# Performance work log

Hardware: AMD Instinct MI355X
Metric: run time of the kernel (lower is better)

## Reference

```python
import jax, jax.numpy as jnp
import numpy as np

H = 512          # hidden_size
B = 1024         # batch
T = 256          # warmup sequence length
NUM_STEPS = 64


def setup_inputs() -> dict:
    key = jax.random.key(0)
    ks = jax.random.split(key, 8)
    bound = 1.0 / np.sqrt(H)  # torch default init for RNN/Linear
    x = jax.random.normal(ks[0], (B, T), dtype=jnp.float32)
    W_ih = jax.random.uniform(ks[1], (H, 1), jnp.float32, -bound, bound)
    W_hh = jax.random.uniform(ks[2], (H, H), jnp.float32, -bound, bound)
    b_ih = jax.random.uniform(ks[3], (H,), jnp.float32, -bound, bound)
    b_hh = jax.random.uniform(ks[4], (H,), jnp.float32, -bound, bound)
    W_fc = jax.random.uniform(ks[5], (1, H), jnp.float32, -bound, bound)
    b_fc = jax.random.uniform(ks[6], (1,), jnp.float32, -bound, bound)
    return {"x": x, "W_ih": W_ih, "W_hh": W_hh, "b_ih": b_ih,
            "b_hh": b_hh, "W_fc": W_fc, "b_fc": b_fc, "num_steps": NUM_STEPS}


def reference(x, W_ih, W_hh, b_ih, b_hh, W_fc, b_fc, num_steps):
    # Phase 1: warmup RNN over the input series. h_t = relu(x_t*W_ih + b_ih + h@W_hh^T + b_hh)
    bias = b_ih + b_hh  # [H]
    w_in = W_ih[:, 0]   # [H], input_size == 1

    def warm_step(h, xt):                      # h: [B,H], xt: [B]
        h = jax.nn.relu(xt[:, None] * w_in[None, :] + h @ W_hh.T + bias)
        return h, None

    h0 = jnp.zeros((B, H), dtype=x.dtype)
    h, _ = jax.lax.scan(warm_step, h0, x.T)    # scan over time: x.T is [T,B]

    def roll_step(h, _):
        y = h @ W_fc.T + b_fc                  # [B,1]
        h = jax.nn.relu(y @ W_ih.T + h @ W_hh.T + bias)
        return h, y

    _, ys = jax.lax.scan(roll_step, h, None, length=num_steps)  # ys: [S,B,1]
    return jnp.transpose(ys, (1, 0, 2))        # [B, num_steps, 1]
```

## Files before the change

kernel.cpp:

```cpp
#include <hip/hip_runtime.h>
#include <stdint.h>

#define H 512
#define B_SZ 1024
#define T_WARM 256
#define NSTEPS 64
#define TOTAL_T (T_WARM + NSTEPS)

#define RPB 16
#define HC 128
#define NTEAM 64
#define NCG 4
#define NBLK 256
#define NTHR 512
#define HSTR 520

typedef __attribute__((ext_vector_type(8))) short bf16x8;
typedef __attribute__((ext_vector_type(4))) float f32x4;

__device__ __forceinline__ ushort f2bf(float f) {
    uint32_t u = __builtin_bit_cast(uint32_t, f);
    u += 0x7FFFu + ((u >> 16) & 1u);
    return (ushort)(u >> 16);
}
__device__ __forceinline__ float bf2f(ushort h) {
    uint32_t u = ((uint32_t)h) << 16;
    return __builtin_bit_cast(float, u);
}

__global__ void prep_kernel(const float* __restrict__ x,
                            const float* __restrict__ W_hh,
                            const float* __restrict__ b_ih,
                            const float* __restrict__ b_hh,
                            ushort* __restrict__ Wh, ushort* __restrict__ Wl,
                            float* __restrict__ bias, float* __restrict__ xT,
                            uint32_t* __restrict__ Hb0, uint32_t* __restrict__ flags) {
    int i = blockIdx.x * NTHR + threadIdx.x;
    Hb0[i] = 0u;
    if (i < 4096) flags[i] = 0u;
    if (i < H * H) {
        float w = W_hh[i];
        ushort hi = f2bf(w);
        float rem = w - bf2f(hi);
        Wh[i] = hi;
        Wl[i] = f2bf(rem);
    }
    if (i < B_SZ * T_WARM) {
        int b = i & (B_SZ - 1), t = i >> 10;
        xT[t * B_SZ + b] = x[b * T_WARM + t];
    }
    if (i < H) bias[i] = b_ih[i] + b_hh[i];
}

__global__ __launch_bounds__(NTHR, 1)
void rnn_kernel(const float* __restrict__ xT,
                const float* __restrict__ W_ih,
                const float* __restrict__ b_fc_p,
                const float* __restrict__ W_fc,
                const ushort* __restrict__ Wh_g,
                const ushort* __restrict__ Wl_g,
                const float* __restrict__ bias_g,
                uint32_t* __restrict__ Hb0, uint32_t* __restrict__ Hb1,
                uint32_t* __restrict__ flags,
                float* __restrict__ out) {
    __shared__ ushort h_hi[RPB * HSTR];
    __shared__ ushort h_lo[RPB * HSTR];
    __shared__ float w_fc_s[H];
    __shared__ float w_in_s[HC];
    __shared__ float bias_s[HC];
    __shared__ float sx[RPB];
    __shared__ float sy[RPB];

    const int tid = threadIdx.x;
    const int bid = blockIdx.x;
    const int team = bid & (NTEAM - 1);
    const int cg = bid >> 6;
    const int row0 = team * RPB;
    const int col0 = cg * HC;

    w_fc_s[tid & (H - 1)] = W_fc[tid & (H - 1)];
    if (tid < HC) { w_in_s[tid] = W_ih[col0 + tid]; bias_s[tid] = bias_g[col0 + tid]; }
    const float bfc = b_fc_p[0];

    const int lane = tid & 63;
    const int wv = tid >> 6;
    const int n = lane & 15, q = lane >> 4;

    bf16x8 Bh[16], Bl[16];
    {
        const ushort* wh = Wh_g + (col0 + wv * 16 + n) * H + q * 8;
        const ushort* wl = Wl_g + (col0 + wv * 16 + n) * H + q * 8;
        #pragma unroll
        for (int kt = 0; kt < 16; ++kt) {
            Bh[kt] = *(const bf16x8*)(wh + kt * 32);
            Bl[kt] = *(const bf16x8*)(wl + kt * 32);
        }
    }

    uint32_t* myflag = flags + (team * NCG + cg) * 16;
    const uint32_t* pollflag = flags + (team * NCG + (wv >> 1)) * 16;

    for (int t = 0; t < TOTAL_T; ++t) {
        float xv = 0.f;
        if (t < T_WARM && tid < RPB) xv = xT[t * B_SZ + row0 + tid];

        if (t > 0) {
            while (__hip_atomic_load(pollflag, __ATOMIC_RELAXED, __HIP_MEMORY_SCOPE_AGENT)
                   < (uint32_t)t)
                __builtin_amdgcn_s_sleep(1);
        }

        uint64_t tmp[8];
        {
            const uint32_t* hb = (t & 1) ? Hb1 : Hb0;
            const uint64_t* src = (const uint64_t*)hb;
            #pragma unroll
            for (int it = 0; it < 8; ++it) {
                int idx = it * 64 + lane;
                int r = idx >> 5, cpair = idx & 31;
                tmp[it] = __hip_atomic_load(src + ((row0 + r) * 256 + wv * 32 + cpair),
                                            __ATOMIC_RELAXED, __HIP_MEMORY_SCOPE_AGENT);
            }
        }
        __syncthreads();

        #pragma unroll
        for (int it = 0; it < 8; ++it) {
            int idx = it * 64 + lane;
            int r = idx >> 5, cpair = idx & 31;
            int k = wv * 64 + cpair * 2;
            uint64_t u = tmp[it];
            uint32_t w0 = (uint32_t)u, w1 = (uint32_t)(u >> 32);
            uint32_t hw = (w0 >> 16) | (w1 & 0xFFFF0000u);
            uint32_t lw = (w0 & 0xFFFFu) | (w1 << 16);
            *(uint32_t*)(&h_hi[r * HSTR + k]) = hw;
            *(uint32_t*)(&h_lo[r * HSTR + k]) = lw;
        }
        if (t < T_WARM && tid < RPB) sx[tid] = xv;
        __syncthreads();

        if (t >= T_WARM) {
            if (tid < RPB * 16) {
                int r = tid >> 4, seg = tid & 15;
                const ushort* hh = &h_hi[r * HSTR];
                const ushort* hl = &h_lo[r * HSTR];
                float s = 0.f;
                #pragma unroll
                for (int kk = 0; kk < 32; ++kk) {
                    int k = seg + kk * 16;
                    s += (bf2f(hh[k]) + bf2f(hl[k])) * w_fc_s[k];
                }
                #pragma unroll
                for (int off = 8; off; off >>= 1) s += __shfl_down(s, off, 16);
                if (seg == 0) {
                    float y = s + bfc;
                    sy[r] = y;
                    if (cg == 0) out[(row0 + r) * NSTEPS + (t - T_WARM)] = y;
                }
            }
            __syncthreads();
        }

        f32x4 acc0 = {0.f, 0.f, 0.f, 0.f}, acc1 = {0.f, 0.f, 0.f, 0.f};
        const ushort* ha = &h_hi[n * HSTR] + q * 8;
        const ushort* la = &h_lo[n * HSTR] + q * 8;
        #pragma unroll
        for (int kt = 0; kt < 16; kt += 2) {
            {
                bf16x8 ah = *(const bf16x8*)(ha + kt * 32);
                bf16x8 al = *(const bf16x8*)(la + kt * 32);
                acc0 = __builtin_amdgcn_mfma_f32_16x16x32_bf16(ah, Bh[kt], acc0, 0, 0, 0);
                acc0 = __builtin_amdgcn_mfma_f32_16x16x32_bf16(al, Bh[kt], acc0, 0, 0, 0);
                acc0 = __builtin_amdgcn_mfma_f32_16x16x32_bf16(ah, Bl[kt], acc0, 0, 0, 0);
            }
            {
                bf16x8 ah = *(const bf16x8*)(ha + (kt + 1) * 32);
                bf16x8 al = *(const bf16x8*)(la + (kt + 1) * 32);
                acc1 = __builtin_amdgcn_mfma_f32_16x16x32_bf16(ah, Bh[kt + 1], acc1, 0, 0, 0);
                acc1 = __builtin_amdgcn_mfma_f32_16x16x32_bf16(al, Bh[kt + 1], acc1, 0, 0, 0);
                acc1 = __builtin_amdgcn_mfma_f32_16x16x32_bf16(ah, Bl[kt + 1], acc1, 0, 0, 0);
            }
        }

        const int jl = wv * 16 + n;
        const float wi = w_in_s[jl], bj = bias_s[jl];
        uint32_t* dst = ((t & 1) ? Hb0 : Hb1) + col0 + jl;
        #pragma unroll
        for (int i = 0; i < 4; ++i) {
            int m = q * 4 + i;
            float sv = (t < T_WARM) ? sx[m] : sy[m];
            float v = acc0[i] + acc1[i] + sv * wi + bj;
            v = fmaxf(v, 0.f);
            ushort hi = f2bf(v);
            float rem = v - bf2f(hi);
            uint32_t u = ((uint32_t)hi << 16) | (uint32_t)f2bf(rem);
            __hip_atomic_store(dst + (row0 + m) * H, u, __ATOMIC_RELAXED, __HIP_MEMORY_SCOPE_AGENT);
        }
        __syncthreads();
        if (tid == 0)
            __hip_atomic_store(myflag, (uint32_t)(t + 1), __ATOMIC_RELAXED, __HIP_MEMORY_SCOPE_AGENT);
    }
}

extern "C" void kernel_launch(void* const* d_in, const int* in_sizes, int n_in,
                              void* d_out, int out_size, void* d_ws, size_t ws_size,
                              hipStream_t stream) {
    const float* x    = (const float*)d_in[0];
    const float* W_ih = (const float*)d_in[1];
    const float* W_hh = (const float*)d_in[2];
    const float* b_ih = (const float*)d_in[3];
    const float* b_hh = (const float*)d_in[4];
    const float* W_fc = (const float*)d_in[5];
    const float* b_fc = (const float*)d_in[6];
    float* out = (float*)d_out;

    uint8_t* w = (uint8_t*)d_ws;
    ushort*   Wh    = (ushort*)(w);
    ushort*   Wl    = (ushort*)(w + 524288);
    float*    bias  = (float*)(w + 1048576);
    float*    xT    = (float*)(w + 1052672);
    uint32_t* Hb0   = (uint32_t*)(w + 2101248);
    uint32_t* Hb1   = (uint32_t*)(w + 4198400);
    uint32_t* flags = (uint32_t*)(w + 6295552);

    prep_kernel<<<1024, NTHR, 0, stream>>>(x, W_hh, b_ih, b_hh, Wh, Wl, bias, xT, Hb0, flags);
    rnn_kernel<<<NBLK, NTHR, 0, stream>>>(xT, W_ih, b_fc, W_fc, Wh, Wl, bias, Hb0, Hb1, flags, out);
}
```

Measured before the change: 1.030 ms.

## Read own column slice from LDS and double-buffer h tiles to drop a barrier

Each block now keeps its freshly computed h slice in a shared-memory staging array, so waves reading their own block's columns skip the flag poll and the global reload. The h_hi/h_lo LDS tiles are double-buffered by step parity, which lets the barrier between the global loads and the LDS writes be removed. The goal is to cut per-step synchronisation and global-memory latency on the serial recurrence critical path. It costs extra LDS, and correctness relies on the end-of-step barrier ordering writes to the staging array.

```diff
diff --git a/kernel.cpp b/kernel.cpp
--- a/kernel.cpp
+++ b/kernel.cpp
@@ -63,8 +63,9 @@
                 uint32_t* __restrict__ Hb0, uint32_t* __restrict__ Hb1,
                 uint32_t* __restrict__ flags,
                 float* __restrict__ out) {
-    __shared__ ushort h_hi[RPB * HSTR];
-    __shared__ ushort h_lo[RPB * HSTR];
+    __shared__ ushort h_hi[2][RPB * HSTR];
+    __shared__ ushort h_lo[2][RPB * HSTR];
+    __shared__ uint32_t tr[RPB * HC];
     __shared__ float w_fc_s[H];
     __shared__ float w_in_s[HC];
     __shared__ float bias_s[HC];
@@ -99,19 +100,28 @@
 
     uint32_t* myflag = flags + (team * NCG + cg) * 16;
     const uint32_t* pollflag = flags + (team * NCG + (wv >> 1)) * 16;
+    const bool selfw = ((wv >> 1) == cg);
 
     for (int t = 0; t < TOTAL_T; ++t) {
         float xv = 0.f;
         if (t < T_WARM && tid < RPB) xv = xT[t * B_SZ + row0 + tid];
 
-        if (t > 0) {
-            while (__hip_atomic_load(pollflag, __ATOMIC_RELAXED, __HIP_MEMORY_SCOPE_AGENT)
-                   < (uint32_t)t)
-                __builtin_amdgcn_s_sleep(1);
-        }
-
         uint64_t tmp[8];
-        {
+        if (t > 0 && selfw) {
+            #pragma unroll
+            for (int it = 0; it < 8; ++it) {
+                int idx = it * 64 + lane;
+                int r = idx >> 5, cpair = idx & 31;
+                int kloc = (wv & 1) * 64 + cpair * 2;
+                const uint32_t* p = &tr[r * HC + kloc];
+                tmp[it] = (uint64_t)p[0] | ((uint64_t)p[1] << 32);
+            }
+        } else {
+            if (t > 0) {
+                while (__hip_atomic_load(pollflag, __ATOMIC_RELAXED, __HIP_MEMORY_SCOPE_AGENT)
+                       < (uint32_t)t)
+                    __builtin_amdgcn_s_sleep(1);
+            }
             const uint32_t* hb = (t & 1) ? Hb1 : Hb0;
             const uint64_t* src = (const uint64_t*)hb;
             #pragma unroll
@@ -122,8 +132,9 @@
                                             __ATOMIC_RELAXED, __HIP_MEMORY_SCOPE_AGENT);
             }
         }
-        __syncthreads();
-
+
+        ushort* hhb = h_hi[t & 1];
+        ushort* hlb = h_lo[t & 1];
         #pragma unroll
         for (int it = 0; it < 8; ++it) {
             int idx = it * 64 + lane;
@@ -133,8 +144,8 @@
             uint32_t w0 = (uint32_t)u, w1 = (uint32_t)(u >> 32);
             uint32_t hw = (w0 >> 16) | (w1 & 0xFFFF0000u);
             uint32_t lw = (w0 & 0xFFFFu) | (w1 << 16);
-            *(uint32_t*)(&h_hi[r * HSTR + k]) = hw;
-            *(uint32_t*)(&h_lo[r * HSTR + k]) = lw;
+            *(uint32_t*)(&hhb[r * HSTR + k]) = hw;
+            *(uint32_t*)(&hlb[r * HSTR + k]) = lw;
         }
         if (t < T_WARM && tid < RPB) sx[tid] = xv;
         __syncthreads();
@@ -142,8 +153,8 @@
         if (t >= T_WARM) {
             if (tid < RPB * 16) {
                 int r = tid >> 4, seg = tid & 15;
-                const ushort* hh = &h_hi[r * HSTR];
-                const ushort* hl = &h_lo[r * HSTR];
+                const ushort* hh = &hhb[r * HSTR];
+                const ushort* hl = &hlb[r * HSTR];
                 float s = 0.f;
                 #pragma unroll
                 for (int kk = 0; kk < 32; ++kk) {
@@ -162,8 +173,8 @@
         }
 
         f32x4 acc0 = {0.f, 0.f, 0.f, 0.f}, acc1 = {0.f, 0.f, 0.f, 0.f};
-        const ushort* ha = &h_hi[n * HSTR] + q * 8;
-        const ushort* la = &h_lo[n * HSTR] + q * 8;
+        const ushort* ha = &hhb[n * HSTR] + q * 8;
+        const ushort* la = &hlb[n * HSTR] + q * 8;
         #pragma unroll
         for (int kt = 0; kt < 16; kt += 2) {
             {
@@ -194,6 +205,7 @@
             ushort hi = f2bf(v);
             float rem = v - bf2f(hi);
             uint32_t u = ((uint32_t)hi << 16) | (uint32_t)f2bf(rem);
+            tr[m * HC + jl] = u;
             __hip_atomic_store(dst + (row0 + m) * H, u, __ATOMIC_RELAXED, __HIP_MEMORY_SCOPE_AGENT);
         }
         __syncthreads();
```

Measured after the change: 1.000 ms. 2.9% less time.

## Split K across waves with hi/lo planes loaded straight into MFMA operands

Applied to the files above, without the earlier changes.

The hidden state is stored in separate bf16 hi and lo global planes, so each wave can atomically load its MFMA A-operands directly from global memory. This removes the repacking into shared memory and the extra barrier that went with it. Work is now split by K: each wave covers 64 K values for all 128 columns, and partial accumulators are reduced through a shared-memory buffer. The fc dot product is computed from the same registers and reduced through shared memory, and the wave whose poll target is its own block skips polling. In exchange it adds an 8-way shared-memory reduction, holds more accumulators in registers, and writes through a lane shuffle to pack hi/lo pairs.

```diff
diff --git a/kernel.cpp b/kernel.cpp
--- a/kernel.cpp
+++ b/kernel.cpp
@@ -13,10 +13,14 @@
 #define NCG 4
 #define NBLK 256
 #define NTHR 512
-#define HSTR 520
 
 typedef __attribute__((ext_vector_type(8))) short bf16x8;
 typedef __attribute__((ext_vector_type(4))) float f32x4;
+
+union u64x2_bf {
+    uint64_t u[2];
+    bf16x8 v;
+};
 
 __device__ __forceinline__ ushort f2bf(float f) {
     uint32_t u = __builtin_bit_cast(uint32_t, f);
@@ -34,9 +38,10 @@
                             const float* __restrict__ b_hh,
                             ushort* __restrict__ Wh, ushort* __restrict__ Wl,
                             float* __restrict__ bias, float* __restrict__ xT,
-                            uint32_t* __restrict__ Hb0, uint32_t* __restrict__ flags) {
-    int i = blockIdx.x * NTHR + threadIdx.x;
-    Hb0[i] = 0u;
+                            uint32_t* __restrict__ Hhi0, uint32_t* __restrict__ Hlo0,
+                            uint32_t* __restrict__ flags) {
+    int i = blockIdx.x * 512 + threadIdx.x;
+    if (i < B_SZ * 256) { Hhi0[i] = 0u; Hlo0[i] = 0u; }
     if (i < 4096) flags[i] = 0u;
     if (i < H * H) {
         float w = W_hh[i];
@@ -60,14 +65,15 @@
                 const ushort* __restrict__ Wh_g,
                 const ushort* __restrict__ Wl_g,
                 const float* __restrict__ bias_g,
-                uint32_t* __restrict__ Hb0, uint32_t* __restrict__ Hb1,
+                uint32_t* __restrict__ Hhi0, uint32_t* __restrict__ Hhi1,
+                uint32_t* __restrict__ Hlo0, uint32_t* __restrict__ Hlo1,
                 uint32_t* __restrict__ flags,
                 float* __restrict__ out) {
-    __shared__ ushort h_hi[RPB * HSTR];
-    __shared__ ushort h_lo[RPB * HSTR];
+    __shared__ float pc[8 * 8 * 64 * 4];
     __shared__ float w_fc_s[H];
     __shared__ float w_in_s[HC];
     __shared__ float bias_s[HC];
+    __shared__ float ypt[32 * 16];
     __shared__ float sx[RPB];
     __shared__ float sy[RPB];
 
@@ -78,7 +84,7 @@
     const int row0 = team * RPB;
     const int col0 = cg * HC;
 
-    w_fc_s[tid & (H - 1)] = W_fc[tid & (H - 1)];
+    w_fc_s[tid] = W_fc[tid];
     if (tid < HC) { w_in_s[tid] = W_ih[col0 + tid]; bias_s[tid] = bias_g[col0 + tid]; }
     const float bfc = b_fc_p[0];
 
@@ -88,113 +94,113 @@
 
     bf16x8 Bh[16], Bl[16];
     {
-        const ushort* wh = Wh_g + (col0 + wv * 16 + n) * H + q * 8;
-        const ushort* wl = Wl_g + (col0 + wv * 16 + n) * H + q * 8;
-        #pragma unroll
-        for (int kt = 0; kt < 16; ++kt) {
-            Bh[kt] = *(const bf16x8*)(wh + kt * 32);
-            Bl[kt] = *(const bf16x8*)(wl + kt * 32);
+        const int kb = wv * 64 + q * 8;
+        #pragma unroll
+        for (int c = 0; c < 8; ++c) {
+            const ushort* wh = Wh_g + (col0 + c * 16 + n) * H + kb;
+            const ushort* wl = Wl_g + (col0 + c * 16 + n) * H + kb;
+            Bh[c * 2 + 0] = *(const bf16x8*)(wh);
+            Bh[c * 2 + 1] = *(const bf16x8*)(wh + 32);
+            Bl[c * 2 + 0] = *(const bf16x8*)(wl);
+            Bl[c * 2 + 1] = *(const bf16x8*)(wl + 32);
         }
     }
 
     uint32_t* myflag = flags + (team * NCG + cg) * 16;
     const uint32_t* pollflag = flags + (team * NCG + (wv >> 1)) * 16;
+    const bool selfw = ((wv >> 1) == cg);
 
     for (int t = 0; t < TOTAL_T; ++t) {
         float xv = 0.f;
         if (t < T_WARM && tid < RPB) xv = xT[t * B_SZ + row0 + tid];
 
-        if (t > 0) {
+        if (t > 0 && !selfw) {
             while (__hip_atomic_load(pollflag, __ATOMIC_RELAXED, __HIP_MEMORY_SCOPE_AGENT)
                    < (uint32_t)t)
                 __builtin_amdgcn_s_sleep(1);
         }
 
-        uint64_t tmp[8];
-        {
-            const uint32_t* hb = (t & 1) ? Hb1 : Hb0;
-            const uint64_t* src = (const uint64_t*)hb;
+        const uint64_t* ph = (const uint64_t*)((t & 1) ? Hhi1 : Hhi0);
+        const uint64_t* pl = (const uint64_t*)((t & 1) ? Hlo1 : Hlo0);
+        const int abase = (row0 + n) * 128 + wv * 16 + q * 2;
+        u64x2_bf ah[2], al[2];
+        #pragma unroll
+        for (int ktl = 0; ktl < 2; ++ktl) {
+            ah[ktl].u[0] = __hip_atomic_load(ph + abase + ktl * 8 + 0, __ATOMIC_RELAXED, __HIP_MEMORY_SCOPE_AGENT);
+            ah[ktl].u[1] = __hip_atomic_load(ph + abase + ktl * 8 + 1, __ATOMIC_RELAXED, __HIP_MEMORY_SCOPE_AGENT);
+            al[ktl].u[0] = __hip_atomic_load(pl + abase + ktl * 8 + 0, __ATOMIC_RELAXED, __HIP_MEMORY_SCOPE_AGENT);
+            al[ktl].u[1] = __hip_atomic_load(pl + abase + ktl * 8 + 1, __ATOMIC_RELAXED, __HIP_MEMORY_SCOPE_AGENT);
+        }
+
+        f32x4 acc[8];
+        #pragma unroll
+        for (int c = 0; c < 8; ++c) acc[c] = (f32x4){0.f, 0.f, 0.f, 0.f};
+        #pragma unroll
+        for (int ktl = 0; ktl < 2; ++ktl) {
             #pragma unroll
-            for (int it = 0; it < 8; ++it) {
-                int idx = it * 64 + lane;
-                int r = idx >> 5, cpair = idx & 31;
-                tmp[it] = __hip_atomic_load(src + ((row0 + r) * 256 + wv * 32 + cpair),
-                                            __ATOMIC_RELAXED, __HIP_MEMORY_SCOPE_AGENT);
+            for (int c = 0; c < 8; ++c) {
+                acc[c] = __builtin_amdgcn_mfma_f32_16x16x32_bf16(ah[ktl].v, Bh[c * 2 + ktl], acc[c], 0, 0, 0);
+                acc[c] = __builtin_amdgcn_mfma_f32_16x16x32_bf16(al[ktl].v, Bh[c * 2 + ktl], acc[c], 0, 0, 0);
+                acc[c] = __builtin_amdgcn_mfma_f32_16x16x32_bf16(ah[ktl].v, Bl[c * 2 + ktl], acc[c], 0, 0, 0);
             }
         }
+
+        #pragma unroll
+        for (int c = 0; c < 8; ++c)
+            *(f32x4*)(&pc[((wv * 8 + c) * 64 + lane) * 4]) = acc[c];
+        if (t < T_WARM && tid < RPB) sx[tid] = xv;
+        if (t >= T_WARM) {
+            float yp = 0.f;
+            #pragma unroll
+            for (int ktl = 0; ktl < 2; ++ktl)
+                #pragma unroll
+                for (int j = 0; j < 8; ++j) {
+                    int k = wv * 64 + ktl * 32 + q * 8 + j;
+                    yp += (bf2f((ushort)ah[ktl].v[j]) + bf2f((ushort)al[ktl].v[j])) * w_fc_s[k];
+                }
+            ypt[(wv * 4 + q) * 16 + n] = yp;
+        }
         __syncthreads();
 
-        #pragma unroll
-        for (int it = 0; it < 8; ++it) {
-            int idx = it * 64 + lane;
-            int r = idx >> 5, cpair = idx & 31;
-            int k = wv * 64 + cpair * 2;
-            uint64_t u = tmp[it];
-            uint32_t w0 = (uint32_t)u, w1 = (uint32_t)(u >> 32);
-            uint32_t hw = (w0 >> 16) | (w1 & 0xFFFF0000u);
-            uint32_t lw = (w0 & 0xFFFFu) | (w1 << 16);
-            *(uint32_t*)(&h_hi[r * HSTR + k]) = hw;
-            *(uint32_t*)(&h_lo[r * HSTR + k]) = lw;
-        }
-        if (t < T_WARM && tid < RPB) sx[tid] = xv;
-        __syncthreads();
-
         if (t >= T_WARM) {
-            if (tid < RPB * 16) {
-                int r = tid >> 4, seg = tid & 15;
-                const ushort* hh = &h_hi[r * HSTR];
-                const ushort* hl = &h_lo[r * HSTR];
-                float s = 0.f;
+            if (tid < RPB) {
+                float s = bfc;
                 #pragma unroll
-                for (int kk = 0; kk < 32; ++kk) {
-                    int k = seg + kk * 16;
-                    s += (bf2f(hh[k]) + bf2f(hl[k])) * w_fc_s[k];
-                }
-                #pragma unroll
-                for (int off = 8; off; off >>= 1) s += __shfl_down(s, off, 16);
-                if (seg == 0) {
-                    float y = s + bfc;
-                    sy[r] = y;
-                    if (cg == 0) out[(row0 + r) * NSTEPS + (t - T_WARM)] = y;
-                }
+                for (int g = 0; g < 32; ++g) s += ypt[g * 16 + tid];
+                sy[tid] = s;
+                if (cg == 0) out[(row0 + tid) * NSTEPS + (t - T_WARM)] = s;
             }
             __syncthreads();
         }
 
-        f32x4 acc0 = {0.f, 0.f, 0.f, 0.f}, acc1 = {0.f, 0.f, 0.f, 0.f};
-        const ushort* ha = &h_hi[n * HSTR] + q * 8;
-        const ushort* la = &h_lo[n * HSTR] + q * 8;
-        #pragma unroll
-        for (int kt = 0; kt < 16; kt += 2) {
-            {
-                bf16x8 ah = *(const bf16x8*)(ha + kt * 32);
-                bf16x8 al = *(const bf16x8*)(la + kt * 32);
-                acc0 = __builtin_amdgcn_mfma_f32_16x16x32_bf16(ah, Bh[kt], acc0, 0, 0, 0);
-                acc0 = __builtin_amdgcn_mfma_f32_16x16x32_bf16(al, Bh[kt], acc0, 0, 0, 0);
-                acc0 = __builtin_amdgcn_mfma_f32_16x16x32_bf16(ah, Bl[kt], acc0, 0, 0, 0);
-            }
-            {
-                bf16x8 ah = *(const bf16x8*)(ha + (kt + 1) * 32);
-                bf16x8 al = *(const bf16x8*)(la + (kt + 1) * 32);
-                acc1 = __builtin_amdgcn_mfma_f32_16x16x32_bf16(ah, Bh[kt + 1], acc1, 0, 0, 0);
-                acc1 = __builtin_amdgcn_mfma_f32_16x16x32_bf16(al, Bh[kt + 1], acc1, 0, 0, 0);
-                acc1 = __builtin_amdgcn_mfma_f32_16x16x32_bf16(ah, Bl[kt + 1], acc1, 0, 0, 0);
-            }
-        }
+        f32x4 v = (f32x4){0.f, 0.f, 0.f, 0.f};
+        #pragma unroll
+        for (int w = 0; w < 8; ++w)
+            v += *(const f32x4*)(&pc[((w * 8 + wv) * 64 + lane) * 4]);
 
         const int jl = wv * 16 + n;
         const float wi = w_in_s[jl], bj = bias_s[jl];
-        uint32_t* dst = ((t & 1) ? Hb0 : Hb1) + col0 + jl;
+        uint32_t* dsth = ((t & 1) ? Hhi0 : Hhi1);
+        uint32_t* dstl = ((t & 1) ? Hlo0 : Hlo1);
+        const int pi = (col0 + jl) >> 1;
         #pragma unroll
         for (int i = 0; i < 4; ++i) {
             int m = q * 4 + i;
             float sv = (t < T_WARM) ? sx[m] : sy[m];
-            float v = acc0[i] + acc1[i] + sv * wi + bj;
-            v = fmaxf(v, 0.f);
-            ushort hi = f2bf(v);
-            float rem = v - bf2f(hi);
-            uint32_t u = ((uint32_t)hi << 16) | (uint32_t)f2bf(rem);
-            __hip_atomic_store(dst + (row0 + m) * H, u, __ATOMIC_RELAXED, __HIP_MEMORY_SCOPE_AGENT);
+            float val = v[i] + sv * wi + bj;
+            val = fmaxf(val, 0.f);
+            ushort hi = f2bf(val);
+            float rem = val - bf2f(hi);
+            uint32_t mine = ((uint32_t)hi << 16) | (uint32_t)f2bf(rem);
+            uint32_t partner = (uint32_t)__shfl_xor((int)mine, 1);
+            int du = (row0 + m) * 256 + pi;
+            if ((n & 1) == 0) {
+                uint32_t hw = (mine >> 16) | (partner & 0xFFFF0000u);
+                __hip_atomic_store(dsth + du, hw, __ATOMIC_RELAXED, __HIP_MEMORY_SCOPE_AGENT);
+            } else {
+                uint32_t lw = (partner & 0xFFFFu) | (mine << 16);
+                __hip_atomic_store(dstl + du, lw, __ATOMIC_RELAXED, __HIP_MEMORY_SCOPE_AGENT);
+            }
         }
         __syncthreads();
         if (tid == 0)
@@ -219,10 +225,13 @@
     ushort*   Wl    = (ushort*)(w + 524288);
     float*    bias  = (float*)(w + 1048576);
     float*    xT    = (float*)(w + 1052672);
-    uint32_t* Hb0   = (uint32_t*)(w + 2101248);
-    uint32_t* Hb1   = (uint32_t*)(w + 4198400);
+    uint32_t* Hhi0  = (uint32_t*)(w + 2101248);
+    uint32_t* Hhi1  = (uint32_t*)(w + 3149824);
+    uint32_t* Hlo0  = (uint32_t*)(w + 4198400);
+    uint32_t* Hlo1  = (uint32_t*)(w + 5246976);
     uint32_t* flags = (uint32_t*)(w + 6295552);
 
-    prep_kernel<<<1024, NTHR, 0, stream>>>(x, W_hh, b_ih, b_hh, Wh, Wl, bias, xT, Hb0, flags);
-    rnn_kernel<<<NBLK, NTHR, 0, stream>>>(xT, W_ih, b_fc, W_fc, Wh, Wl, bias, Hb0, Hb1, flags, out);
-}
+    prep_kernel<<<1024, 512, 0, stream>>>(x, W_hh, b_ih, b_hh, Wh, Wl, bias, xT, Hhi0, Hlo0, flags);
+    rnn_kernel<<<NBLK, NTHR, 0, stream>>>(xT, W_ih, b_fc, W_fc, Wh, Wl, bias,
+                                          Hhi0, Hhi1, Hlo0, Hlo1, flags, out);
+}
```

Measured after the change: 1.173 ms. +13.8%, slower.
